# Kernel tuning notes

Measured on AMD Instinct MI355X. Metric: run time of the kernel, lower is better.

The kernel has to match this reference:

```python
import jax, jax.numpy as jnp
import numpy as np

DIM = 384
HEADS = 8
SR = 2
BN_EPS = 1e-5


def setup_inputs() -> dict:
    key = jax.random.key(0)
    ks = jax.random.split(key, 8)
    B, Hh, Ww = 4, 64, 64
    N = Hh * Ww
    Nk = (Hh // SR) * (Ww // SR)
    w = lambda k, s: jax.random.normal(k, s, jnp.float32) * 0.02
    return {
        "x": jax.random.normal(ks[0], (B, N, DIM), jnp.float32),
        "relative_pos": jax.random.normal(ks[1], (HEADS, N, Nk), jnp.float32) * 0.02,
        "H": Hh,
        "W": Ww,
        "Wq": w(ks[2], (DIM, DIM)),
        "Wk": w(ks[3], (DIM, DIM)),
        "Wv": w(ks[4], (DIM, DIM)),
        "Wp": w(ks[5], (DIM, DIM)),
        "bp": jnp.zeros((DIM,), jnp.float32),
        "sr_w": w(ks[6], (DIM, 1, SR, SR)),  # depthwise conv, OIHW with groups=DIM
        "sr_b": jnp.zeros((DIM,), jnp.float32),
        "bn_gamma": jnp.ones((DIM,), jnp.float32),
        "bn_beta": jnp.zeros((DIM,), jnp.float32),
        "bn_mean": jnp.zeros((DIM,), jnp.float32),
        "bn_var": jnp.ones((DIM,), jnp.float32),
    }


def reference(x, relative_pos, Wq, Wk, Wv, Wp, bp, sr_w, sr_b,
              bn_gamma, bn_beta, bn_mean, bn_var, H, W):
    B, N, C = x.shape
    hd = C // HEADS
    scale = hd ** (-0.5)
    # q projection -> [B, heads, N, hd]
    q = (x @ Wq.T).reshape(B, N, HEADS, hd).transpose(0, 2, 1, 3)
    # spatial reduction: depthwise conv stride SR + BatchNorm (eval mode)
    x_ = x.transpose(0, 2, 1).reshape(B, C, H, W)
    y = jax.lax.conv_general_dilated(
        x_, sr_w, window_strides=(SR, SR), padding="VALID",
        feature_group_count=C,
        dimension_numbers=("NCHW", "OIHW", "NCHW"))
    y = y + sr_b[None, :, None, None]
    inv = jax.lax.rsqrt(bn_var + BN_EPS) * bn_gamma
    y = (y - bn_mean[None, :, None, None]) * inv[None, :, None, None] \
        + bn_beta[None, :, None, None]
    xk = y.reshape(B, C, -1).transpose(0, 2, 1)  # [B, Nk, C]
    Nk = xk.shape[1]
    k = (xk @ Wk.T).reshape(B, Nk, HEADS, hd).transpose(0, 2, 1, 3)
    v = (xk @ Wv.T).reshape(B, Nk, HEADS, hd).transpose(0, 2, 1, 3)
    # scores with additive relative-position bias (broadcast over batch)
    attn = jnp.einsum("bhnd,bhmd->bhnm", q, k) * scale + relative_pos
    attn = jax.nn.softmax(attn, axis=-1)
    out = jnp.einsum("bhnm,bhmd->bhnd", attn, v)
    out = out.transpose(0, 2, 1, 3).reshape(B, N, C)
    return out @ Wp.T + bp
```

## Files before the change

### kernel.cpp

```cpp
#include <hip/hip_runtime.h>
#include <hip/hip_bf16.h>

#define LOG2E 1.4426950408889634f

typedef short bf16x8 __attribute__((ext_vector_type(8)));
typedef float f32x4  __attribute__((ext_vector_type(4)));

#define OFF_BPf  16
#define OFF_SRWf (OFF_BPf + 384)
#define OFF_SRBf (OFF_SRWf + 1536)
#define OFF_GAf  (OFF_SRBf + 384)
#define OFF_BEf  (OFF_GAf + 384)
#define OFF_MUf  (OFF_BEf + 384)
#define OFF_VAf  (OFF_MUf + 384)
#define U_XB 7712
#define U_WQ (U_XB + 6291456)
#define U_WK (U_WQ + 147456)
#define U_WV (U_WK + 147456)
#define U_WP (U_WV + 147456)
#define U_XK (U_WP + 147456)
#define U_QB (U_XK + 1572864)
#define U_KB (U_QB + 6291456)
#define U_VT (U_KB + 1572864)
#define U_OB (U_VT + 1572864)

static __device__ __forceinline__ float bfu(unsigned short u){ return __uint_as_float(((unsigned)u) << 16); }
static __device__ __forceinline__ float bf_lo(unsigned v){ return __uint_as_float(v << 16); }
static __device__ __forceinline__ float bf_hi(unsigned v){ return __uint_as_float(v & 0xFFFF0000u); }
static __device__ __forceinline__ unsigned short f2bf(float f){
  unsigned u = __float_as_uint(f);
  u += 0x7FFFu + ((u >> 16) & 1u);
  return (unsigned short)(u >> 16);
}
static __device__ __forceinline__ unsigned pkcvt(float a, float b){
  float2 f; f.x = a; f.y = b;
  __hip_bfloat162 h = __float22bfloat162_rn(f);
  union { __hip_bfloat162 h2; unsigned u; } cv; cv.h2 = h; return cv.u;
}
static __device__ __forceinline__ unsigned pk2bf(float a, float b){
  return pkcvt(a, b);
}
static __device__ __forceinline__ float fast_exp2(float x){ return __builtin_amdgcn_exp2f(x); }
static __device__ __forceinline__ void gld_lds16(const void* g, void* l){
  __builtin_amdgcn_global_load_lds((const __attribute__((address_space(1))) void*)g,
                                   (__attribute__((address_space(3))) void*)l, 16, 0, 0);
}

__global__ void detect_bf16(const unsigned* __restrict__ xraw, int* __restrict__ flag){
  unsigned w = xraw[threadIdx.x];
  unsigned e = (w >> 7) & 0xFFu;
  unsigned long long m = __ballot(e >= 118u && e <= 137u);
  if (threadIdx.x == 0) *flag = (__popcll(m) >= 40) ? 1 : 0;
}

static __device__ __forceinline__ void cp8_bf(unsigned short* dst, const void* src, int off, bool bf){
  if (bf) { *(uint4*)dst = *(const uint4*)((const unsigned short*)src + off); }
  else {
    const float* s = (const float*)src + off;
    float4 a = *(const float4*)s, b = *(const float4*)(s + 4);
    uint4 o; o.x = pk2bf(a.x, a.y); o.y = pk2bf(a.z, a.w);
    o.z = pk2bf(b.x, b.y); o.w = pk2bf(b.z, b.w);
    *(uint4*)dst = o;
  }
}
static __device__ __forceinline__ void cp8_f(float* dst, const void* src, int off, bool bf){
  if (bf) {
    const unsigned short* s = (const unsigned short*)src + off;
    uint4 w = *(const uint4*)s;
    float4 a, b;
    a.x = bf_lo(w.x); a.y = bf_hi(w.x); a.z = bf_lo(w.y); a.w = bf_hi(w.y);
    b.x = bf_lo(w.z); b.y = bf_hi(w.z); b.z = bf_lo(w.w); b.w = bf_hi(w.w);
    *(float4*)dst = a; *(float4*)(dst + 4) = b;
  } else {
    const float* s = (const float*)src + off;
    *(float4*)dst = *(const float4*)s;
    *(float4*)(dst + 4) = *(const float4*)(s + 4);
  }
}

__global__ __launch_bounds__(256) void convert_all(
    const void* x, const void* wq, const void* wk, const void* wv, const void* wp,
    const void* bp, const void* srw, const void* srb, const void* ga, const void* be,
    const void* mu, const void* va, float* ws){
  const bool bf = ((const int*)ws)[0] != 0;
  unsigned short* u = (unsigned short*)ws;
  int g = blockIdx.x * 256 + threadIdx.x;
  if (g < 786432) { cp8_bf(u + U_XB + g*8, x,  g*8, bf); return; }  g -= 786432;
  if (g < 18432)  { cp8_bf(u + U_WQ + g*8, wq, g*8, bf); return; }  g -= 18432;
  if (g < 18432)  { cp8_bf(u + U_WK + g*8, wk, g*8, bf); return; }  g -= 18432;
  if (g < 18432)  { cp8_bf(u + U_WV + g*8, wv, g*8, bf); return; }  g -= 18432;
  if (g < 18432)  { cp8_bf(u + U_WP + g*8, wp, g*8, bf); return; }  g -= 18432;
  if (g < 192)    { cp8_f(ws + OFF_SRWf + g*8, srw, g*8, bf); return; } g -= 192;
  if (g < 48)     { cp8_f(ws + OFF_BPf  + g*8, bp,  g*8, bf); return; } g -= 48;
  if (g < 48)     { cp8_f(ws + OFF_SRBf + g*8, srb, g*8, bf); return; } g -= 48;
  if (g < 48)     { cp8_f(ws + OFF_GAf  + g*8, ga,  g*8, bf); return; } g -= 48;
  if (g < 48)     { cp8_f(ws + OFF_BEf  + g*8, be,  g*8, bf); return; } g -= 48;
  if (g < 48)     { cp8_f(ws + OFF_MUf  + g*8, mu,  g*8, bf); return; } g -= 48;
  if (g < 48)     { cp8_f(ws + OFF_VAf  + g*8, va,  g*8, bf); }
}

__global__ __launch_bounds__(256) void sr_bn(const unsigned short* __restrict__ xb,
    const float* __restrict__ wsf, unsigned short* __restrict__ xkb){
  int idx = blockIdx.x * 256 + threadIdx.x;
  int c8 = idx % 48;
  int nk = (idx / 48) & 1023;
  int b  = idx / (48 * 1024);
  int i = nk >> 5, j = nk & 31;
  int c0 = c8 * 8;
  const unsigned short* xp = xb + ((size_t)(b*4096 + i*128 + j*2))*384 + c0;
  unsigned aw[4], bw[4], cw[4], dw[4];
  *(uint4*)aw = *(const uint4*)(xp);
  *(uint4*)bw = *(const uint4*)(xp + 384);
  *(uint4*)cw = *(const uint4*)(xp + 64*384);
  *(uint4*)dw = *(const uint4*)(xp + 65*384);
  unsigned out[4];
  #pragma unroll
  for (int k2 = 0; k2 < 4; ++k2) {
    float r2[2];
    #pragma unroll
    for (int half = 0; half < 2; ++half) {
      int k = k2*2 + half;
      int c = c0 + k;
      float xa = half ? bf_hi(aw[k2]) : bf_lo(aw[k2]);
      float xbv = half ? bf_hi(bw[k2]) : bf_lo(bw[k2]);
      float xc = half ? bf_hi(cw[k2]) : bf_lo(cw[k2]);
      float xd = half ? bf_hi(dw[k2]) : bf_lo(dw[k2]);
      float acc = xa*wsf[OFF_SRWf+c*4] + xbv*wsf[OFF_SRWf+c*4+1]
                + xc*wsf[OFF_SRWf+c*4+2] + xd*wsf[OFF_SRWf+c*4+3];
      float inv = rsqrtf(wsf[OFF_VAf+c] + 1e-5f) * wsf[OFF_GAf+c];
      r2[half] = (acc + wsf[OFF_SRBf+c] - wsf[OFF_MUf+c]) * inv + wsf[OFF_BEf+c];
    }
    out[k2] = pkcvt(r2[0], r2[1]);
  }
  *(uint4*)(xkb + (size_t)idx*8) = *(uint4*)out;
}

__global__ __launch_bounds__(512) void proj_qkv(unsigned short* __restrict__ u){
  int z, by;
  if (blockIdx.y < 128)      { z = 0; by = blockIdx.y; }
  else if (blockIdx.y < 160) { z = 1; by = blockIdx.y - 128; }
  else                       { z = 2; by = blockIdx.y - 160; }
  const unsigned short* A = u + ((z == 0) ? U_XB : U_XK);
  const unsigned short* W = u + ((z == 0) ? U_WQ : (z == 1) ? U_WK : U_WV);

  __shared__ unsigned short As[128][40];
  __shared__ unsigned short Ws[128][40];
  const int tid = threadIdx.x;
  const int wave = tid >> 6, lane = tid & 63, lg = lane >> 4, ln = lane & 15;
  const int m0 = by * 128, n0 = blockIdx.x * 128;
  const int wm = (wave >> 2) * 64, wn = (wave & 3) * 32;
  f32x4 acc[4][2];
  #pragma unroll
  for (int i = 0; i < 4; ++i)
    #pragma unroll
    for (int j = 0; j < 2; ++j) acc[i][j] = (f32x4){0.f,0.f,0.f,0.f};

  const int arow = tid >> 2, acol = (tid & 3) * 8;
  for (int kt = 0; kt < 384; kt += 32) {
    uint4 a0 = *(const uint4*)&A[(size_t)(m0+arow)*384 + kt + acol];
    uint4 w0 = *(const uint4*)&W[(size_t)(n0+arow)*384 + kt + acol];
    __syncthreads();
    *(uint4*)&As[arow][acol] = a0;
    *(uint4*)&Ws[arow][acol] = w0;
    __syncthreads();
    bf16x8 af[4], wf[2];
    #pragma unroll
    for (int mi = 0; mi < 4; ++mi) af[mi] = *(const bf16x8*)&As[wm + mi*16 + ln][lg*8];
    #pragma unroll
    for (int ni = 0; ni < 2; ++ni) wf[ni] = *(const bf16x8*)&Ws[wn + ni*16 + ln][lg*8];
    #pragma unroll
    for (int mi = 0; mi < 4; ++mi)
      #pragma unroll
      for (int ni = 0; ni < 2; ++ni)
        acc[mi][ni] = __builtin_amdgcn_mfma_f32_16x16x32_bf16(af[mi], wf[ni], acc[mi][ni], 0, 0, 0);
  }

  unsigned short* outQ = u + U_QB;
  unsigned short* outK = u + U_KB;
  unsigned short* outV = u + U_VT;
  #pragma unroll
  for (int mi = 0; mi < 4; ++mi)
    #pragma unroll
    for (int ni = 0; ni < 2; ++ni) {
      int gcol = n0 + wn + ni*16 + ln;
      if (z == 2) {
        int grow0 = m0 + wm + mi*16 + lg*4;
        int hh = gcol / 48, d = gcol - hh*48;
        int bb = grow0 >> 10, mk = grow0 & 1023;
        uint2 st; st.x = pkcvt(acc[mi][ni][0], acc[mi][ni][1]);
        st.y = pkcvt(acc[mi][ni][2], acc[mi][ni][3]);
        *(uint2*)&outV[((size_t)((bb*8 + hh)*48 + d))*1024 + mk] = st;
      } else {
        unsigned short* dst = (z == 0) ? outQ : outK;
        #pragma unroll
        for (int r = 0; r < 4; ++r) {
          int grow = m0 + wm + mi*16 + lg*4 + r;
          dst[(size_t)grow*384 + gcol] = f2bf(acc[mi][ni][r]);
        }
      }
    }
}

__global__ __launch_bounds__(512) void gemm_out(const unsigned short* __restrict__ A,
    const unsigned short* __restrict__ W, const float* __restrict__ bias,
    void* __restrict__ out, const int* __restrict__ flag){
  __shared__ unsigned short As[128][40];
  __shared__ unsigned short Ws[128][40];
  const int tid = threadIdx.x;
  const int wave = tid >> 6, lane = tid & 63, lg = lane >> 4, ln = lane & 15;
  const int m0 = blockIdx.y * 128, n0 = blockIdx.x * 128;
  const int wm = (wave >> 2) * 64, wn = (wave & 3) * 32;
  f32x4 acc[4][2];
  #pragma unroll
  for (int i = 0; i < 4; ++i)
    #pragma unroll
    for (int j = 0; j < 2; ++j) acc[i][j] = (f32x4){0.f,0.f,0.f,0.f};

  const int arow = tid >> 2, acol = (tid & 3) * 8;
  for (int kt = 0; kt < 384; kt += 32) {
    uint4 a0 = *(const uint4*)&A[(size_t)(m0+arow)*384 + kt + acol];
    uint4 w0 = *(const uint4*)&W[(size_t)(n0+arow)*384 + kt + acol];
    __syncthreads();
    *(uint4*)&As[arow][acol] = a0;
    *(uint4*)&Ws[arow][acol] = w0;
    __syncthreads();
    bf16x8 af[4], wf[2];
    #pragma unroll
    for (int mi = 0; mi < 4; ++mi) af[mi] = *(const bf16x8*)&As[wm + mi*16 + ln][lg*8];
    #pragma unroll
    for (int ni = 0; ni < 2; ++ni) wf[ni] = *(const bf16x8*)&Ws[wn + ni*16 + ln][lg*8];
    #pragma unroll
    for (int mi = 0; mi < 4; ++mi)
      #pragma unroll
      for (int ni = 0; ni < 2; ++ni)
        acc[mi][ni] = __builtin_amdgcn_mfma_f32_16x16x32_bf16(af[mi], wf[ni], acc[mi][ni], 0, 0, 0);
  }

  const bool bff = (*flag != 0);
  #pragma unroll
  for (int mi = 0; mi < 4; ++mi)
    #pragma unroll
    for (int ni = 0; ni < 2; ++ni)
      #pragma unroll
      for (int r = 0; r < 4; ++r) {
        int grow = m0 + wm + mi*16 + lg*4 + r;
        int gcol = n0 + wn + ni*16 + ln;
        float v = acc[mi][ni][r] + bias[gcol];
        if (bff) ((unsigned short*)out)[(size_t)grow*384 + gcol] = f2bf(v);
        else     ((float*)out)[(size_t)grow*384 + gcol] = v;
      }
}

__global__ __launch_bounds__(256, 4) void attn_mfma(const unsigned short* __restrict__ qb,
    const unsigned short* __restrict__ kb, const unsigned short* __restrict__ vt,
    const void* __restrict__ rel, const int* __restrict__ flag,
    unsigned short* __restrict__ ob){
  __shared__ __align__(16) unsigned short Kbuf[2][6*512];
  __shared__ __align__(16) unsigned short Vbuf[8*384];
  __shared__ __align__(16) unsigned short Ps[4][16][64];
  __shared__ float Ls[4][32];
  const int x = blockIdx.x;
  const int b = x >> 5, nb = x & 31, h = blockIdx.y;
  const int tid = threadIdx.x, wave = tid >> 6, lane = tid & 63;
  const int lg = lane >> 4, ln = lane & 15;
  const int qrow0 = nb * 128 + wave * 32;
  const bool bfm = (*flag != 0);
  const float SCL = 0.14433756729740643f * LOG2E;

  bf16x8 qf0[2], qf1[2];
  #pragma unroll
  for (int qt = 0; qt < 2; ++qt) {
    const unsigned short* qp = qb + ((size_t)(b*4096 + qrow0 + qt*16 + ln))*384 + h*48;
    qf0[qt] = *(const bf16x8*)(qp + lg*8);
    bf16x8 z = {0,0,0,0,0,0,0,0};
    if (lg < 2) z = *(const bf16x8*)(qp + 32 + lg*8);
    qf1[qt] = z;
  }

  f32x4 o[2][3];
  #pragma unroll
  for (int qt = 0; qt < 2; ++qt) { o[qt][0] = (f32x4){0.f,0.f,0.f,0.f}; o[qt][1] = o[qt][0]; o[qt][2] = o[qt][0]; }
  float lsum[2] = {0.f, 0.f};

  const float* relf = (const float*)rel;
  const unsigned short* relh = (const unsigned short*)rel;
  const size_t rbase = ((size_t)(h*4096 + qrow0 + ln)) * 1024;
  const size_t kbase = (size_t)(b*1024) * 384 + (size_t)h*48;
  const size_t vbase = ((size_t)(b*8 + h)) * 48 * 1024;

  const unsigned swz = (unsigned)((ln & 7) << 4);
  char* psrow = (char*)&Ps[wave][ln][0];

  const int jk1 = wave;
  const int jk2 = 4 + wave;
  const int jv1 = wave;
  const int jv2 = 2 + wave;
  int s1i = jv1*64 + lane;  int c1 = s1i/48, d1 = s1i - 48*c1;
  size_t vg1 = vbase + (size_t)d1*1024 + c1*8;
  int s2i = jv2*64 + lane;  int c2 = s2i/48, d2 = s2i - 48*c2;
  size_t vg2 = vbase + (size_t)d2*1024 + c2*8;

  gld_lds16(kb + kbase + (size_t)lane*384 + jk1*8, &Kbuf[0][jk1*512]);
  if (wave < 2) gld_lds16(kb + kbase + (size_t)lane*384 + jk2*8, &Kbuf[0][jk2*512]);

  #pragma unroll 1
  for (int t = 0; t < 16; ++t) {
    const int cbuf = t & 1, nbuf = cbuf ^ 1;
    __syncthreads();

    uint2 rr[2][4];
    if (bfm) {
      #pragma unroll
      for (int qt = 0; qt < 2; ++qt)
        #pragma unroll
        for (int mt = 0; mt < 4; ++mt)
          rr[qt][mt] = *(const uint2*)(relh + rbase + (size_t)qt*16384 + t*64 + mt*16 + lg*4);
    } else {
      #pragma unroll
      for (int qt = 0; qt < 2; ++qt)
        #pragma unroll
        for (int mt = 0; mt < 4; ++mt) {
          float4 q_ = *(const float4*)(relf + rbase + (size_t)qt*16384 + t*64 + mt*16 + lg*4);
          rr[qt][mt].x = pkcvt(q_.x, q_.y); rr[qt][mt].y = pkcvt(q_.z, q_.w);
        }
    }

    gld_lds16(vt + vg1 + t*64, &Vbuf[jv1*512]);
    if (wave >= 2) gld_lds16(vt + vg2 + t*64, &Vbuf[jv2*512]);
    const int T = (t + 1 < 16) ? t + 1 : 15;
    gld_lds16(kb + kbase + (size_t)T*24576 + (size_t)lane*384 + jk1*8, &Kbuf[nbuf][jk1*512]);
    if (wave < 2) gld_lds16(kb + kbase + (size_t)T*24576 + (size_t)lane*384 + jk2*8, &Kbuf[nbuf][jk2*512]);

    f32x4 s0[4];
    #pragma unroll
    for (int mt = 0; mt < 4; ++mt) {
      bf16x8 k0 = *(const bf16x8*)&Kbuf[cbuf][lg*512 + (mt*16 + ln)*8];
      bf16x8 k1 = {0,0,0,0,0,0,0,0};
      if (lg < 2) k1 = *(const bf16x8*)&Kbuf[cbuf][(4 + lg)*512 + (mt*16 + ln)*8];
      s0[mt] = __builtin_amdgcn_mfma_f32_16x16x32_bf16(k0, qf0[0], (f32x4){0.f,0.f,0.f,0.f}, 0, 0, 0);
      s0[mt] = __builtin_amdgcn_mfma_f32_16x16x32_bf16(k1, qf1[0], s0[mt], 0, 0, 0);
    }
    {
      float lacc = 0.f;
      #pragma unroll
      for (int mt = 0; mt < 4; ++mt) {
        float r0 = bf_lo(rr[0][mt].x), r1 = bf_hi(rr[0][mt].x);
        float r2 = bf_lo(rr[0][mt].y), r3 = bf_hi(rr[0][mt].y);
        float p0 = fast_exp2(fmaf(s0[mt][0], SCL, r0 * LOG2E));
        float p1 = fast_exp2(fmaf(s0[mt][1], SCL, r1 * LOG2E));
        float p2 = fast_exp2(fmaf(s0[mt][2], SCL, r2 * LOG2E));
        float p3 = fast_exp2(fmaf(s0[mt][3], SCL, r3 * LOG2E));
        lacc += (p0 + p1) + (p2 + p3);
        uint2 w; w.x = pkcvt(p0, p1); w.y = pkcvt(p2, p3);
        *(uint2*)(psrow + (((unsigned)(mt*32 + lg*8)) ^ swz)) = w;
      }
      lsum[0] += lacc;
    }

    __syncthreads();

    #pragma unroll
    for (int ks = 0; ks < 2; ++ks) {
      bf16x8 vf[3];
      #pragma unroll
      for (int nd = 0; nd < 3; ++nd)
        vf[nd] = *(const bf16x8*)&Vbuf[(ks*4 + lg)*384 + (nd*16 + ln)*8];
      bf16x8 pa = *(const bf16x8*)(psrow + (((unsigned)(ks*64 + lg*16)) ^ swz));
      #pragma unroll
      for (int nd = 0; nd < 3; ++nd)
        o[0][nd] = __builtin_amdgcn_mfma_f32_16x16x32_bf16(pa, vf[nd], o[0][nd], 0, 0, 0);
    }

    f32x4 s1[4];
    #pragma unroll
    for (int mt = 0; mt < 4; ++mt) {
      bf16x8 k0 = *(const bf16x8*)&Kbuf[cbuf][lg*512 + (mt*16 + ln)*8];
      bf16x8 k1 = {0,0,0,0,0,0,0,0};
      if (lg < 2) k1 = *(const bf16x8*)&Kbuf[cbuf][(4 + lg)*512 + (mt*16 + ln)*8];
      s1[mt] = __builtin_amdgcn_mfma_f32_16x16x32_bf16(k0, qf0[1], (f32x4){0.f,0.f,0.f,0.f}, 0, 0, 0);
      s1[mt] = __builtin_amdgcn_mfma_f32_16x16x32_bf16(k1, qf1[1], s1[mt], 0, 0, 0);
    }
    {
      float lacc = 0.f;
      #pragma unroll
      for (int mt = 0; mt < 4; ++mt) {
        float r0 = bf_lo(rr[1][mt].x), r1 = bf_hi(rr[1][mt].x);
        float r2 = bf_lo(rr[1][mt].y), r3 = bf_hi(rr[1][mt].y);
        float p0 = fast_exp2(fmaf(s1[mt][0], SCL, r0 * LOG2E));
        float p1 = fast_exp2(fmaf(s1[mt][1], SCL, r1 * LOG2E));
        float p2 = fast_exp2(fmaf(s1[mt][2], SCL, r2 * LOG2E));
        float p3 = fast_exp2(fmaf(s1[mt][3], SCL, r3 * LOG2E));
        lacc += (p0 + p1) + (p2 + p3);
        uint2 w; w.x = pkcvt(p0, p1); w.y = pkcvt(p2, p3);
        *(uint2*)(psrow + (((unsigned)(mt*32 + lg*8)) ^ swz)) = w;
      }
      lsum[1] += lacc;
    }
    #pragma unroll
    for (int ks = 0; ks < 2; ++ks) {
      bf16x8 vf[3];
      #pragma unroll
      for (int nd = 0; nd < 3; ++nd)
        vf[nd] = *(const bf16x8*)&Vbuf[(ks*4 + lg)*384 + (nd*16 + ln)*8];
      bf16x8 pa = *(const bf16x8*)(psrow + (((unsigned)(ks*64 + lg*16)) ^ swz));
      #pragma unroll
      for (int nd = 0; nd < 3; ++nd)
        o[1][nd] = __builtin_amdgcn_mfma_f32_16x16x32_bf16(pa, vf[nd], o[1][nd], 0, 0, 0);
    }
  }

  #pragma unroll
  for (int qt = 0; qt < 2; ++qt) {
    lsum[qt] += __shfl_xor(lsum[qt], 16, 64);
    lsum[qt] += __shfl_xor(lsum[qt], 32, 64);
    if (lg == 0) Ls[wave][qt*16 + ln] = lsum[qt];
  }
  #pragma unroll
  for (int qt = 0; qt < 2; ++qt)
    #pragma unroll
    for (int r = 0; r < 4; ++r) {
      float l = Ls[wave][qt*16 + lg*4 + r];
      float linv = 1.0f / l;
      size_t rowb = ((size_t)(b*4096 + qrow0 + qt*16 + lg*4 + r))*384 + h*48 + ln;
      #pragma unroll
      for (int nd = 0; nd < 3; ++nd)
        ob[rowb + nd*16] = f2bf(o[qt][nd][r] * linv);
    }
}

extern "C" void kernel_launch(void* const* d_in, const int* in_sizes, int n_in,
                              void* d_out, int out_size, void* d_ws, size_t ws_size,
                              hipStream_t stream) {
  float* ws = (float*)d_ws;
  int* flag = (int*)d_ws;
  unsigned short* u = (unsigned short*)d_ws;

  detect_bf16<<<1, 64, 0, stream>>>((const unsigned*)d_in[0], flag);
  convert_all<<<3363, 256, 0, stream>>>(d_in[0], d_in[4], d_in[5], d_in[6], d_in[7],
      d_in[8], d_in[9], d_in[10], d_in[11], d_in[12], d_in[13], d_in[14], ws);
  sr_bn<<<768, 256, 0, stream>>>(u + U_XB, ws, u + U_XK);
  proj_qkv<<<dim3(3, 192), 512, 0, stream>>>(u);
  attn_mfma<<<dim3(128, 8), 256, 0, stream>>>(u + U_QB, u + U_KB, u + U_VT, d_in[1], flag, u + U_OB);
  gemm_out<<<dim3(3, 128), 512, 0, stream>>>(u + U_OB, u + U_WP, ws + OFF_BPf, d_out, flag);
}
```

Baseline: 350.6 us.

## Double-buffer projection GEMMs with direct global-to-LDS async loads

Rewrites the main loop of the QKV projection and output projection GEMMs to use a helper (gld_lds16, presumably global-to-LDS direct loads) into double-buffered shared memory with a k-major layout. The next K-slice is prefetched while MFMAs consume the current buffer, and one barrier per iteration replaces two. The aim is to hide global load latency and drop the register round trip through VGPRs. Correctness depends on the helper's wait semantics before the barrier, and the new unpadded layout may change LDS bank conflicts.

```diff
diff --git a/kernel.cpp b/kernel.cpp
--- a/kernel.cpp
+++ b/kernel.cpp
@@ -143,8 +143,8 @@
   const unsigned short* A = u + ((z == 0) ? U_XB : U_XK);
   const unsigned short* W = u + ((z == 0) ? U_WQ : (z == 1) ? U_WK : U_WV);
 
-  __shared__ unsigned short As[128][40];
-  __shared__ unsigned short Ws[128][40];
+  __shared__ __align__(16) unsigned short As[2][4096];
+  __shared__ __align__(16) unsigned short Ws[2][4096];
   const int tid = threadIdx.x;
   const int wave = tid >> 6, lane = tid & 63, lg = lane >> 4, ln = lane & 15;
   const int m0 = by * 128, n0 = blockIdx.x * 128;
@@ -155,19 +155,28 @@
     #pragma unroll
     for (int j = 0; j < 2; ++j) acc[i][j] = (f32x4){0.f,0.f,0.f,0.f};
 
-  const int arow = tid >> 2, acol = (tid & 3) * 8;
-  for (int kt = 0; kt < 384; kt += 32) {
-    uint4 a0 = *(const uint4*)&A[(size_t)(m0+arow)*384 + kt + acol];
-    uint4 w0 = *(const uint4*)&W[(size_t)(n0+arow)*384 + kt + acol];
+  const int jj = wave >> 1, hh2 = wave & 1;
+  const int srow = hh2*64 + lane;
+  const size_t agb = (size_t)(m0 + srow)*384 + jj*8;
+  const size_t wgb = (size_t)(n0 + srow)*384 + jj*8;
+  const int lds_off = jj*1024 + hh2*512;
+
+  gld_lds16(A + agb, &As[0][lds_off]);
+  gld_lds16(W + wgb, &Ws[0][lds_off]);
+
+  #pragma unroll 1
+  for (int i = 0; i < 12; ++i) {
+    const int cb = i & 1, nb2 = cb ^ 1;
     __syncthreads();
-    *(uint4*)&As[arow][acol] = a0;
-    *(uint4*)&Ws[arow][acol] = w0;
-    __syncthreads();
+    if (i + 1 < 12) {
+      gld_lds16(A + agb + (i+1)*32, &As[nb2][lds_off]);
+      gld_lds16(W + wgb + (i+1)*32, &Ws[nb2][lds_off]);
+    }
     bf16x8 af[4], wf[2];
     #pragma unroll
-    for (int mi = 0; mi < 4; ++mi) af[mi] = *(const bf16x8*)&As[wm + mi*16 + ln][lg*8];
-    #pragma unroll
-    for (int ni = 0; ni < 2; ++ni) wf[ni] = *(const bf16x8*)&Ws[wn + ni*16 + ln][lg*8];
+    for (int mi = 0; mi < 4; ++mi) af[mi] = *(const bf16x8*)&As[cb][lg*1024 + (wm + mi*16 + ln)*8];
+    #pragma unroll
+    for (int ni = 0; ni < 2; ++ni) wf[ni] = *(const bf16x8*)&Ws[cb][lg*1024 + (wn + ni*16 + ln)*8];
     #pragma unroll
     for (int mi = 0; mi < 4; ++mi)
       #pragma unroll
@@ -204,8 +213,8 @@
 __global__ __launch_bounds__(512) void gemm_out(const unsigned short* __restrict__ A,
     const unsigned short* __restrict__ W, const float* __restrict__ bias,
     void* __restrict__ out, const int* __restrict__ flag){
-  __shared__ unsigned short As[128][40];
-  __shared__ unsigned short Ws[128][40];
+  __shared__ __align__(16) unsigned short As[2][4096];
+  __shared__ __align__(16) unsigned short Ws[2][4096];
   const int tid = threadIdx.x;
   const int wave = tid >> 6, lane = tid & 63, lg = lane >> 4, ln = lane & 15;
   const int m0 = blockIdx.y * 128, n0 = blockIdx.x * 128;
@@ -216,19 +225,28 @@
     #pragma unroll
     for (int j = 0; j < 2; ++j) acc[i][j] = (f32x4){0.f,0.f,0.f,0.f};
 
-  const int arow = tid >> 2, acol = (tid & 3) * 8;
-  for (int kt = 0; kt < 384; kt += 32) {
-    uint4 a0 = *(const uint4*)&A[(size_t)(m0+arow)*384 + kt + acol];
-    uint4 w0 = *(const uint4*)&W[(size_t)(n0+arow)*384 + kt + acol];
+  const int jj = wave >> 1, hh2 = wave & 1;
+  const int srow = hh2*64 + lane;
+  const size_t agb = (size_t)(m0 + srow)*384 + jj*8;
+  const size_t wgb = (size_t)(n0 + srow)*384 + jj*8;
+  const int lds_off = jj*1024 + hh2*512;
+
+  gld_lds16(A + agb, &As[0][lds_off]);
+  gld_lds16(W + wgb, &Ws[0][lds_off]);
+
+  #pragma unroll 1
+  for (int i = 0; i < 12; ++i) {
+    const int cb = i & 1, nb2 = cb ^ 1;
     __syncthreads();
-    *(uint4*)&As[arow][acol] = a0;
-    *(uint4*)&Ws[arow][acol] = w0;
-    __syncthreads();
+    if (i + 1 < 12) {
+      gld_lds16(A + agb + (i+1)*32, &As[nb2][lds_off]);
+      gld_lds16(W + wgb + (i+1)*32, &Ws[nb2][lds_off]);
+    }
     bf16x8 af[4], wf[2];
     #pragma unroll
-    for (int mi = 0; mi < 4; ++mi) af[mi] = *(const bf16x8*)&As[wm + mi*16 + ln][lg*8];
-    #pragma unroll
-    for (int ni = 0; ni < 2; ++ni) wf[ni] = *(const bf16x8*)&Ws[wn + ni*16 + ln][lg*8];
+    for (int mi = 0; mi < 4; ++mi) af[mi] = *(const bf16x8*)&As[cb][lg*1024 + (wm + mi*16 + ln)*8];
+    #pragma unroll
+    for (int ni = 0; ni < 2; ++ni) wf[ni] = *(const bf16x8*)&Ws[cb][lg*1024 + (wn + ni*16 + ln)*8];
     #pragma unroll
     for (int mi = 0; mi < 4; ++mi)
       #pragma unroll
```

Result: slower. 359.5 us (+2.5%).
